# Kernel optimization log

Measured on AMD Instinct MI355X. Metric: run time of the kernel, lower is better.

Reference implementation:

```python
import jax, jax.numpy as jnp
import numpy as np

K = 2          # downsample rate
H = 8          # attention heads
D_LLM = 1024
DK = D_LLM // H
N_LAYER = 2
F_HID = D_LLM // 4  # 256, per PositionwiseFeedForward(llm_dim, llm_dim//4)
EPS = 1e-12


def _ln(x, g, b):
    m = jnp.mean(x, axis=-1, keepdims=True)
    v = jnp.mean((x - m) ** 2, axis=-1, keepdims=True)
    return (x - m) * jax.lax.rsqrt(v + EPS) * g + b


def setup_inputs() -> dict:
    key = jax.random.key(0)
    ks = jax.random.split(key, 16)
    s = 0.02
    d_in = 512 * K   # encoder_dim * k = 1024
    d_ff = 2048
    inp = {
        'x':  jax.random.normal(ks[0], (8, 2048, 512), dtype=jnp.float32),
        'W1': jax.random.normal(ks[1], (d_ff, d_in)) * s,
        'b1': jnp.zeros((d_ff,)),
        'W2': jax.random.normal(ks[2], (D_LLM, d_ff)) * s,
        'b2': jnp.zeros((D_LLM,)),
        'ln1_g': jnp.ones((N_LAYER, D_LLM)), 'ln1_b': jnp.zeros((N_LAYER, D_LLM)),
        'ln2_g': jnp.ones((N_LAYER, D_LLM)), 'ln2_b': jnp.zeros((N_LAYER, D_LLM)),
        'Wq': jax.random.normal(ks[3], (N_LAYER, D_LLM, D_LLM)) * s, 'bq': jnp.zeros((N_LAYER, D_LLM)),
        'Wk': jax.random.normal(ks[4], (N_LAYER, D_LLM, D_LLM)) * s, 'bk': jnp.zeros((N_LAYER, D_LLM)),
        'Wv': jax.random.normal(ks[5], (N_LAYER, D_LLM, D_LLM)) * s, 'bv': jnp.zeros((N_LAYER, D_LLM)),
        'Wo': jax.random.normal(ks[6], (N_LAYER, D_LLM, D_LLM)) * s, 'bo': jnp.zeros((N_LAYER, D_LLM)),
        'Fw1': jax.random.normal(ks[7], (N_LAYER, F_HID, D_LLM)) * s, 'Fb1': jnp.zeros((N_LAYER, F_HID)),
        'Fw2': jax.random.normal(ks[8], (N_LAYER, D_LLM, F_HID)) * s, 'Fb2': jnp.zeros((N_LAYER, D_LLM)),
    }
    return inp


def reference(x, W1, b1, W2, b2, ln1_g, ln1_b, ln2_g, ln2_b,
              Wq, bq, Wk, bk, Wv, bv, Wo, bo, Fw1, Fb1, Fw2, Fb2):
    B, S, D = x.shape
    chunk = (S - 1) // K + 1
    pad = chunk * K - S
    x = jnp.pad(x, ((0, 0), (0, pad), (0, 0)))
    x = x.reshape(B, chunk, K * D)                    # [B, T, k*D]
    # downsample projection: linear2(relu(linear1(x)))
    x = jax.nn.relu(x @ W1.T + b1) @ W2.T + b2        # [B, T, D_LLM]
    T = chunk
    for l in range(N_LAYER):
        # --- self-attention sublayer (pre-norm) ---
        resid = x
        h = _ln(x, ln1_g[l], ln1_b[l])
        q = (h @ Wq[l].T + bq[l]).reshape(B, T, H, DK).transpose(0, 2, 1, 3)
        k_ = (h @ Wk[l].T + bk[l]).reshape(B, T, H, DK).transpose(0, 2, 1, 3)
        v = (h @ Wv[l].T + bv[l]).reshape(B, T, H, DK).transpose(0, 2, 1, 3)
        scores = jnp.einsum('bhqd,bhkd->bhqk', q, k_) * (DK ** -0.5)
        attn = jax.nn.softmax(scores, axis=-1)        # mask is None
        o = jnp.einsum('bhqk,bhkd->bhqd', attn, v)
        o = o.transpose(0, 2, 1, 3).reshape(B, T, H * DK)
        x = resid + o @ Wo[l].T + bo[l]
        # --- FFN sublayer (pre-norm) ---
        resid = x
        h = _ln(x, ln2_g[l], ln2_b[l])
        x = resid + jax.nn.relu(h @ Fw1[l].T + Fb1[l]) @ Fw2[l].T + Fb2[l]
    return x
```

## Files before the change

### kernel.cpp

```cpp
#include <hip/hip_runtime.h>
#include <hip/hip_bf16.h>


#define DMODEL 1024
#define DFF 2048
#define FHID 256
#define NHEAD 8
#define DKH 128
#define TSEQ 1024

typedef __hip_bfloat16 bf16;
typedef __attribute__((ext_vector_type(8))) short bf16x8;
typedef __attribute__((ext_vector_type(4))) float f32x4;

#define MFMA16(a, b, c) __builtin_amdgcn_mfma_f32_16x16x32_bf16(a, b, c, 0, 0, 0)

__device__ int g_is_bf16;

__device__ __forceinline__ bool flagbf() {
    return __hip_atomic_load(&g_is_bf16, __ATOMIC_ACQUIRE,
                             __HIP_MEMORY_SCOPE_AGENT) != 0;
}
__device__ __forceinline__ bool flagbf_block() {
    __shared__ int fsh;
    if (threadIdx.x == 0)
        fsh = __hip_atomic_load(&g_is_bf16, __ATOMIC_ACQUIRE,
                                __HIP_MEMORY_SCOPE_AGENT);
    __syncthreads();
    return fsh != 0;
}
__device__ __forceinline__ float gload(const void* p, size_t i, bool bf) {
    return bf ? __bfloat162float(((const bf16*)p)[i]) : ((const float*)p)[i];
}
__device__ __forceinline__ void gstore(void* p, size_t i, bool bf, float v) {
    if (bf) ((bf16*)p)[i] = __float2bfloat16(v);
    else    ((float*)p)[i] = v;
}

__device__ __forceinline__ void async16(const bf16* g, const bf16* l) {
    __builtin_amdgcn_global_load_lds(
        (const __attribute__((address_space(1))) void*)g,
        (__attribute__((address_space(3))) void*)l, 16, 0, 0);
}

__global__ void detect_kernel(const void* __restrict__ probe) {
    const int lane = threadIdx.x & 63;
    const bf16* h = (const bf16*)probe;
    int ok = 1;
    #pragma unroll
    for (int j = 0; j < 4; ++j) {
        float v = __bfloat162float(h[lane * 4 + j]);
        if (!(fabsf(v) <= 1000.0f)) ok = 0;
    }
    unsigned long long m = __ballot(ok);
    if (lane == 0)
        __hip_atomic_store(&g_is_bf16, m == ~0ull ? 1 : 0, __ATOMIC_RELEASE,
                           __HIP_MEMORY_SCOPE_AGENT);
}

#define O_W1  0ull
#define O_W2  2097152ull
#define O_QK  4194304ull
#define O_WV  8388608ull
#define O_WO  10485760ull
#define O_F1  12582912ull
#define O_F2  13107200ull
#define ARENA_ELEMS 13631488ull

__global__ __launch_bounds__(256) void cvt_weights(
        const void* W1, const void* W2, const void* Wq, const void* Wk,
        const void* Wv, const void* Wo, const void* F1, const void* F2,
        bf16* __restrict__ arena) {
    if (flagbf_block()) return;
    int b = blockIdx.x;
    const float* src; bf16* dst;
    if      (b < 128)  {           src = (const float*)W1 + (size_t)b * 16384;
                         dst = arena + O_W1 + (size_t)b * 16384; }
    else if (b < 256)  { b -= 128; src = (const float*)W2 + (size_t)b * 16384;
                         dst = arena + O_W2 + (size_t)b * 16384; }
    else if (b < 384)  { b -= 256; src = (const float*)Wq + (size_t)b * 16384;
                         dst = arena + O_QK + (size_t)(b >> 6) * 2097152
                                            + (size_t)(b & 63) * 16384; }
    else if (b < 512)  { b -= 384; src = (const float*)Wk + (size_t)b * 16384;
                         dst = arena + O_QK + (size_t)(b >> 6) * 2097152
                                            + 1048576 + (size_t)(b & 63) * 16384; }
    else if (b < 640)  { b -= 512; src = (const float*)Wv + (size_t)b * 16384;
                         dst = arena + O_WV + (size_t)b * 16384; }
    else if (b < 768)  { b -= 640; src = (const float*)Wo + (size_t)b * 16384;
                         dst = arena + O_WO + (size_t)b * 16384; }
    else if (b < 800)  { b -= 768; src = (const float*)F1 + (size_t)b * 16384;
                         dst = arena + O_F1 + (size_t)b * 16384; }
    else               { b -= 800; src = (const float*)F2 + (size_t)b * 16384;
                         dst = arena + O_F2 + (size_t)b * 16384; }
    const int tid = threadIdx.x;
    #pragma unroll
    for (int it = 0; it < 16; ++it) {
        const int e = it * 1024 + tid * 4;
        float4 f = *(const float4*)(src + e);
        bf16 t[4] = {__float2bfloat16(f.x), __float2bfloat16(f.y),
                     __float2bfloat16(f.z), __float2bfloat16(f.w)};
        *(uint2*)(dst + e) = *(const uint2*)t;
    }
}

__global__ __launch_bounds__(256) void cvt_x(
        const void* __restrict__ X, size_t x_off, bf16* __restrict__ dst) {
    if (flagbf_block()) return;
    const float* src = (const float*)X + x_off + (size_t)blockIdx.x * 16384;
    bf16* d = dst + (size_t)blockIdx.x * 16384;
    const int tid = threadIdx.x;
    #pragma unroll
    for (int it = 0; it < 16; ++it) {
        const int e = it * 1024 + tid * 4;
        float4 f = *(const float4*)(src + e);
        bf16 t[4] = {__float2bfloat16(f.x), __float2bfloat16(f.y),
                     __float2bfloat16(f.z), __float2bfloat16(f.w)};
        *(uint2*)(d + e) = *(const uint2*)t;
    }
}

template <bool RELU, bool ADD, int CMODE, bool TRANSC, bool BIAS2>
__global__ __launch_bounds__(256) void gemm_bf16(
        const bf16* Abf, const bf16* Acv,
        const bf16* Wlo_bf, const bf16* Whi_bf,
        const bf16* Wlo_cv, const bf16* Whi_cv,
        const void* __restrict__ bias, const void* __restrict__ bias2,
        size_t b_off,
        void* __restrict__ C, size_t c_off,
        int M, int N, int K) {
    const bool fl = flagbf_block();
    const bf16* A   = fl ? Abf : Acv;
    const bf16* Wlo = fl ? Wlo_bf : Wlo_cv;
    const bf16* Whi = fl ? Whi_bf : Whi_cv;

    __shared__ __align__(16) bf16 As[128 * 64];
    __shared__ __align__(16) bf16 Bs[128 * 64];

    const int gx = gridDim.x;
    const int lin = blockIdx.x + gx * blockIdx.y;
    const int xcd = lin & 7, j = lin >> 3;
    const int rpx = gridDim.y >> 3;
    const int bm = (xcd * rpx + j / gx) * 128;
    const int bn = (j % gx) * 128;

    const int tid = threadIdx.x;
    const int wave = tid >> 6, lane = tid & 63;
    const int quad = lane >> 4, l15 = lane & 15;
    const int wr = wave >> 1, wc = wave & 1;
    const int l8 = lane >> 3, l7 = lane & 7;
    const int swz = l7 ^ l8;

    const bf16* Wp;
    int bnr;
    if (BIAS2 && bn >= 1024) { Wp = Whi; bnr = bn - 1024; }
    else                     { Wp = Wlo; bnr = bn; }

    f32x4 acc[4][4];
    #pragma unroll
    for (int i = 0; i < 4; ++i)
        #pragma unroll
        for (int j2 = 0; j2 < 4; ++j2) acc[i][j2] = (f32x4){0.f, 0.f, 0.f, 0.f};

    const bf16* ga0 = A  + (size_t)(bm  + wave * 32 + l8) * K + swz * 8;
    const bf16* gb0 = Wp + (size_t)(bnr + wave * 32 + l8) * K + swz * 8;
    bf16* la0 = &As[(wave * 32) * 64];
    bf16* lb0 = &Bs[(wave * 32) * 64];

    for (int k0 = 0; k0 < K; k0 += 64) {
        __syncthreads();
        #pragma unroll
        for (int i = 0; i < 4; ++i) {
            async16(ga0 + (size_t)(i * 8) * K + k0, la0 + i * 512);
            async16(gb0 + (size_t)(i * 8) * K + k0, lb0 + i * 512);
        }
        __syncthreads();

        #pragma unroll
        for (int ks = 0; ks < 2; ++ks) {
            bf16x8 af[4], bfr[4];
            #pragma unroll
            for (int mi = 0; mi < 4; ++mi) {
                const int row = wr * 64 + mi * 16 + l15;
                af[mi] = *(const bf16x8*)
                    &As[row * 64 + ((((ks << 2) | quad) ^ (row & 7)) << 3)];
            }
            #pragma unroll
            for (int ni = 0; ni < 4; ++ni) {
                const int row = wc * 64 + ni * 16 + l15;
                bfr[ni] = *(const bf16x8*)
                    &Bs[row * 64 + ((((ks << 2) | quad) ^ (row & 7)) << 3)];
            }
            #pragma unroll
            for (int mi = 0; mi < 4; ++mi)
                #pragma unroll
                for (int ni = 0; ni < 4; ++ni)
                    acc[mi][ni] = MFMA16(af[mi], bfr[ni], acc[mi][ni]);
        }
    }

    const bool cbf = CMODE ? fl : true;
    #pragma unroll
    for (int ni = 0; ni < 4; ++ni) {
        const int col = bn + wc * 64 + ni * 16 + l15;
        float bv;
        if (BIAS2) bv = col < 1024 ? gload(bias, b_off + col, fl)
                                   : gload(bias2, b_off + col - 1024, fl);
        else       bv = gload(bias, b_off + col, fl);
        #pragma unroll
        for (int mi = 0; mi < 4; ++mi) {
            const int row0 = bm + wr * 64 + mi * 16 + quad * 4;
            if (TRANSC) {
                bf16 pk[4];
                #pragma unroll
                for (int rr = 0; rr < 4; ++rr)
                    pk[rr] = __float2bfloat16(acc[mi][ni][rr] + bv);
                *(uint2*)((bf16*)C + c_off + (size_t)col * M + row0) =
                    *(const uint2*)pk;
            } else {
                #pragma unroll
                for (int rr = 0; rr < 4; ++rr) {
                    float v = acc[mi][ni][rr] + bv;
                    if (RELU) v = fmaxf(v, 0.f);
                    size_t idx = c_off + (size_t)(row0 + rr) * N + col;
                    if (ADD) v += gload(C, idx, cbf);
                    gstore(C, idx, cbf, v);
                }
            }
        }
    }
}

__global__ __launch_bounds__(256) void ln_wave(
        const void* __restrict__ X, size_t x_off,
        const void* __restrict__ g, const void* __restrict__ b, size_t gb_off,
        bf16* __restrict__ H) {
    const bool fl = flagbf_block();
    const int lane = threadIdx.x & 63;
    const int row = blockIdx.x * 4 + (threadIdx.x >> 6);
    const size_t xrow = x_off + (size_t)row * DMODEL;

    float v[16];
    if (fl) {
        const bf16* xp = (const bf16*)X + xrow;
        #pragma unroll
        for (int c = 0; c < 2; ++c) {
            uint4 raw = *(const uint4*)(xp + c * 512 + lane * 8);
            const bf16* rb = (const bf16*)&raw;
            #pragma unroll
            for (int j = 0; j < 8; ++j) v[c * 8 + j] = __bfloat162float(rb[j]);
        }
    } else {
        const float* xp = (const float*)X + xrow;
        #pragma unroll
        for (int c = 0; c < 4; ++c) {
            float4 f = *(const float4*)(xp + c * 256 + lane * 4);
            v[c * 4 + 0] = f.x; v[c * 4 + 1] = f.y;
            v[c * 4 + 2] = f.z; v[c * 4 + 3] = f.w;
        }
    }

    float s = 0.f;
    #pragma unroll
    for (int j = 0; j < 16; ++j) s += v[j];
    #pragma unroll
    for (int off = 32; off > 0; off >>= 1) s += __shfl_xor(s, off);
    const float mean = s * (1.f / DMODEL);

    float vs = 0.f;
    #pragma unroll
    for (int j = 0; j < 16; ++j) { float d = v[j] - mean; vs += d * d; }
    #pragma unroll
    for (int off = 32; off > 0; off >>= 1) vs += __shfl_xor(vs, off);
    const float rstd = rsqrtf(vs * (1.f / DMODEL) + 1e-12f);

    bf16* h = H + (size_t)row * DMODEL;
    if (fl) {
        const bf16* gp = (const bf16*)g + gb_off;
        const bf16* bp = (const bf16*)b + gb_off;
        #pragma unroll
        for (int c = 0; c < 2; ++c) {
            const int o = c * 512 + lane * 8;
            uint4 gr = *(const uint4*)(gp + o);
            uint4 br = *(const uint4*)(bp + o);
            const bf16* gg = (const bf16*)&gr;
            const bf16* bb = (const bf16*)&br;
            bf16 outv[8];
            #pragma unroll
            for (int j = 0; j < 8; ++j)
                outv[j] = __float2bfloat16((v[c * 8 + j] - mean) * rstd *
                          __bfloat162float(gg[j]) + __bfloat162float(bb[j]));
            *(uint4*)(h + o) = *(const uint4*)outv;
        }
    } else {
        const float* gp = (const float*)g + gb_off;
        const float* bp = (const float*)b + gb_off;
        #pragma unroll
        for (int c = 0; c < 4; ++c) {
            const int o = c * 256 + lane * 4;
            float4 gr = *(const float4*)(gp + o);
            float4 br = *(const float4*)(bp + o);
            const float gg[4] = {gr.x, gr.y, gr.z, gr.w};
            const float bb[4] = {br.x, br.y, br.z, br.w};
            bf16 outv[4];
            #pragma unroll
            for (int j = 0; j < 4; ++j)
                outv[j] = __float2bfloat16((v[c * 4 + j] - mean) * rstd * gg[j] + bb[j]);
            *(uint2*)(h + o) = *(const uint2*)outv;
        }
    }
}

__global__ __launch_bounds__(512) void attn_mfma(
        const bf16* __restrict__ QK, const bf16* __restrict__ Vg,
        bf16* __restrict__ Om) {
    const int cch = (int)gridDim.z;
    const int lin = blockIdx.x + (int)gridDim.x *
                    (blockIdx.y + (int)gridDim.y * blockIdx.z);
    const int xcd = lin & 7, j = lin >> 3;
    const int qt = j & 7, gl = j >> 3;
    const int g = xcd * cch + gl;
    const int h = g & 7, bb = g >> 3;

    const int Mc = cch * TSEQ;
    const int tid = threadIdx.x;
    const int wave = tid >> 6, lane = tid & 63;
    const int quad = lane >> 4, l15 = lane & 15;

    __shared__ __align__(16) bf16 Kt[64][128];
    __shared__ __align__(16) bf16 Vt[128][64];
    __shared__ __align__(16) bf16 Ps[8][16][72];

    const int qrow = qt * 128 + wave * 16 + l15;
    const float scale = 0.08838834764831845f;

    bf16x8 qf[4];
    #pragma unroll
    for (int kc = 0; kc < 4; ++kc) {
        uint4 raw = *(const uint4*)(QK + (size_t)(bb * TSEQ + qrow) * 2048 +
                                    h * DKH + kc * 32 + quad * 8);
        const bf16* rb = (const bf16*)&raw;
        bf16 tmp[8];
        #pragma unroll
        for (int j2 = 0; j2 < 8; ++j2)
            tmp[j2] = __float2bfloat16(__bfloat162float(rb[j2]) * scale);
        qf[kc] = *(const bf16x8*)tmp;
    }

    f32x4 o[8];
    #pragma unroll
    for (int i = 0; i < 8; ++i) o[i] = (f32x4){0.f, 0.f, 0.f, 0.f};
    float m_i[4] = {-1e30f, -1e30f, -1e30f, -1e30f};
    float l_i[4] = {0.f, 0.f, 0.f, 0.f};

    const int skey = tid >> 3;
    const int dseg = (tid & 7) * 16;
    const int sk7 = skey & 7;
    const int vd = tid >> 2;
    const int vseg = (tid & 3) * 16;

    for (int kt = 0; kt < TSEQ / 64; ++kt) {
        __syncthreads();
        {
            const bf16* kp = QK + (size_t)(bb * TSEQ + kt * 64 + skey) * 2048 +
                             1024 + h * DKH + dseg;
            const bf16* vp = Vg + (size_t)(h * DKH + vd) * Mc + bb * TSEQ +
                             kt * 64 + vseg;
            uint4 kv[2], vv[2];
            #pragma unroll
            for (int g2 = 0; g2 < 2; ++g2) { kv[g2] = ((const uint4*)kp)[g2]; vv[g2] = ((const uint4*)vp)[g2]; }
            #pragma unroll
            for (int g2 = 0; g2 < 2; ++g2) {
                int c = (dseg >> 3) + g2;
                *(uint4*)&Kt[skey][(c ^ sk7) << 3] = kv[g2];
            }
            #pragma unroll
            for (int g2 = 0; g2 < 2; ++g2) {
                int c = (vseg >> 3) + g2;
                *(uint4*)&Vt[vd][(c ^ (vd & 7)) << 3] = vv[g2];
            }
        }
        __syncthreads();

        f32x4 s[4];
        #pragma unroll
        for (int ni = 0; ni < 4; ++ni) s[ni] = (f32x4){0.f, 0.f, 0.f, 0.f};
        #pragma unroll
        for (int ni = 0; ni < 4; ++ni) {
            const int key = ni * 16 + l15;
            #pragma unroll
            for (int kc = 0; kc < 4; ++kc) {
                const int d3 = kc * 4 + quad;
                bf16x8 kb = *(const bf16x8*)&Kt[key][(d3 ^ (key & 7)) << 3];
                s[ni] = MFMA16(qf[kc], kb, s[ni]);
            }
        }

        float tm[4], ts[4];
        #pragma unroll
        for (int rr = 0; rr < 4; ++rr) {
            float v = fmaxf(fmaxf(s[0][rr], s[1][rr]), fmaxf(s[2][rr], s[3][rr]));
            v = fmaxf(v, __shfl_xor(v, 1));
            v = fmaxf(v, __shfl_xor(v, 2));
            v = fmaxf(v, __shfl_xor(v, 4));
            v = fmaxf(v, __shfl_xor(v, 8));
            tm[rr] = v;
        }
        int grow = 0;
        #pragma unroll
        for (int rr = 0; rr < 4; ++rr)
            grow |= (tm[rr] > m_i[rr] + 8.f) ? 1 : 0;
        if (__any(grow)) {
            float al[4];
            #pragma unroll
            for (int rr = 0; rr < 4; ++rr) {
                float mn = fmaxf(m_i[rr], tm[rr]);
                al[rr] = __expf(m_i[rr] - mn);
                m_i[rr] = mn;
                l_i[rr] *= al[rr];
            }
            #pragma unroll
            for (int i = 0; i < 8; ++i)
                #pragma unroll
                for (int rr = 0; rr < 4; ++rr) o[i][rr] *= al[rr];
        }
        #pragma unroll
        for (int rr = 0; rr < 4; ++rr) ts[rr] = 0.f;
        #pragma unroll
        for (int ni = 0; ni < 4; ++ni)
            #pragma unroll
            for (int rr = 0; rr < 4; ++rr) {
                float p = __expf(s[ni][rr] - m_i[rr]);
                s[ni][rr] = p;
                ts[rr] += p;
            }
        #pragma unroll
        for (int rr = 0; rr < 4; ++rr) {
            float v = ts[rr];
            v += __shfl_xor(v, 1);
            v += __shfl_xor(v, 2);
            v += __shfl_xor(v, 4);
            v += __shfl_xor(v, 8);
            l_i[rr] += v;
        }

        #pragma unroll
        for (int ni = 0; ni < 4; ++ni)
            #pragma unroll
            for (int rr = 0; rr < 4; ++rr)
                Ps[wave][quad * 4 + rr][ni * 16 + l15] = __float2bfloat16(s[ni][rr]);
        __asm__ __volatile__("s_waitcnt lgkmcnt(0)" ::: "memory");
        bf16x8 pa[2];
        #pragma unroll
        for (int kc2 = 0; kc2 < 2; ++kc2)
            pa[kc2] = *(const bf16x8*)&Ps[wave][l15][kc2 * 32 + quad * 8];

        #pragma unroll
        for (int ni2 = 0; ni2 < 8; ++ni2) {
            const int d = ni2 * 16 + l15;
            #pragma unroll
            for (int kc2 = 0; kc2 < 2; ++kc2) {
                const int key3 = kc2 * 4 + quad;
                bf16x8 vb = *(const bf16x8*)&Vt[d][(key3 ^ (d & 7)) << 3];
                o[ni2] = MFMA16(pa[kc2], vb, o[ni2]);
            }
        }
    }

    float rinv[4];
    #pragma unroll
    for (int rr = 0; rr < 4; ++rr) rinv[rr] = 1.0f / l_i[rr];
    const size_t obase = (size_t)bb * TSEQ * DMODEL + (size_t)h * DKH;
    #pragma unroll
    for (int ni2 = 0; ni2 < 8; ++ni2)
        #pragma unroll
        for (int rr = 0; rr < 4; ++rr) {
            int qr = qt * 128 + wave * 16 + quad * 4 + rr;
            Om[obase + (size_t)qr * DMODEL + ni2 * 16 + l15] =
                __float2bfloat16(o[ni2][rr] * rinv[rr]);
        }
}

extern "C" void kernel_launch(void* const* d_in, const int* in_sizes, int n_in,
                              void* d_out, int out_size, void* d_ws, size_t ws_size,
                              hipStream_t stream) {
    const void* x     = d_in[0];
    const void* W1    = d_in[1];
    const void* b1    = d_in[2];
    const void* W2    = d_in[3];
    const void* b2    = d_in[4];
    const void* ln1_g = d_in[5];
    const void* ln1_b = d_in[6];
    const void* ln2_g = d_in[7];
    const void* ln2_b = d_in[8];
    const void* Wq    = d_in[9];
    const void* bq    = d_in[10];
    const void* Wk    = d_in[11];
    const void* bk    = d_in[12];
    const void* Wv    = d_in[13];
    const void* bv    = d_in[14];
    const void* Wo    = d_in[15];
    const void* bo    = d_in[16];
    const void* Fw1   = d_in[17];
    const void* Fb1   = d_in[18];
    const void* Fw2   = d_in[19];
    const void* Fb2   = d_in[20];

    detect_kernel<<<1, 64, 0, stream>>>(W1);

    int c = 8;
    while (c > 1 &&
           (5ull * (size_t)c * (1ull << 20) + ARENA_ELEMS) * 2ull > ws_size)
        c >>= 1;
    const int nch = 8 / c;
    const int Mc = c * TSEQ;
    const size_t SL = (size_t)Mc * DMODEL;

    bf16* Hh  = (bf16*)d_ws;
    bf16* QKb = Hh + SL;
    bf16* Vtb = QKb + 2 * SL;
    bf16* Xc  = Vtb + SL;
    bf16* Wt  = Xc + SL;
    bf16* Hid = QKb;
    bf16* Ffh = QKb;
    bf16* Ob  = Hh;
    void* X = d_out;

    const bf16* xb  = (const bf16*)x;
    bf16* cW1  = Wt + O_W1;
    bf16* cW2  = Wt + O_W2;
    bf16* cWqk = Wt + O_QK;
    bf16* cWv  = Wt + O_WV;
    bf16* cWo  = Wt + O_WO;
    bf16* cF1  = Wt + O_F1;
    bf16* cF2  = Wt + O_F2;

    cvt_weights<<<832, 256, 0, stream>>>(W1, W2, Wq, Wk, Wv, Wo, Fw1, Fw2, Wt);

    for (int ci = 0; ci < nch; ++ci) {
        const size_t roff = (size_t)ci * Mc * DMODEL;

        cvt_x<<<(int)(SL / 16384), 256, 0, stream>>>(x, roff, Xc);

        gemm_bf16<true, false, 0, false, false><<<dim3(DFF / 128, Mc / 128), 256, 0, stream>>>(
            xb + roff, Xc, (const bf16*)W1, (const bf16*)W1, cW1, cW1,
            b1, nullptr, 0, Hid, 0, Mc, DFF, DMODEL);
        gemm_bf16<false, false, 1, false, false><<<dim3(DMODEL / 128, Mc / 128), 256, 0, stream>>>(
            Hid, Hid, (const bf16*)W2, (const bf16*)W2, cW2, cW2,
            b2, nullptr, 0, X, roff, Mc, DMODEL, DFF);

        for (int l = 0; l < 2; ++l) {
            const size_t wOff   = (size_t)l * DMODEL * DMODEL;
            const size_t fOff   = (size_t)l * FHID * DMODEL;
            const size_t vOff   = (size_t)l * DMODEL;
            const size_t f1bOff = (size_t)l * FHID;

            const bf16* wqL = (const bf16*)Wq + wOff;
            const bf16* wkL = (const bf16*)Wk + wOff;
            const bf16* wvL = (const bf16*)Wv + wOff;
            const bf16* woL = (const bf16*)Wo + wOff;
            const bf16* f1L = (const bf16*)Fw1 + fOff;
            const bf16* f2L = (const bf16*)Fw2 + fOff;
            const bf16* qkLo = cWqk + (size_t)l * 2097152;
            const bf16* qkHi = qkLo + 1048576;

            ln_wave<<<Mc / 4, 256, 0, stream>>>(X, roff, ln1_g, ln1_b, vOff, Hh);
            gemm_bf16<false, false, 0, false, true><<<dim3(2048 / 128, Mc / 128), 256, 0, stream>>>(
                Hh, Hh, wqL, wkL, qkLo, qkHi,
                bq, bk, vOff, QKb, 0, Mc, 2048, DMODEL);
            gemm_bf16<false, false, 0, true, false><<<dim3(DMODEL / 128, Mc / 128), 256, 0, stream>>>(
                Hh, Hh, wvL, wvL, cWv + wOff, cWv + wOff,
                bv, nullptr, vOff, Vtb, 0, Mc, DMODEL, DMODEL);

            attn_mfma<<<dim3(TSEQ / 128, NHEAD, c), 512, 0, stream>>>(QKb, Vtb, Ob);

            gemm_bf16<false, true, 1, false, false><<<dim3(DMODEL / 128, Mc / 128), 256, 0, stream>>>(
                Ob, Ob, woL, woL, cWo + wOff, cWo + wOff,
                bo, nullptr, vOff, X, roff, Mc, DMODEL, DMODEL);

            ln_wave<<<Mc / 4, 256, 0, stream>>>(X, roff, ln2_g, ln2_b, vOff, Hh);
            gemm_bf16<true, false, 0, false, false><<<dim3(FHID / 128, Mc / 128), 256, 0, stream>>>(
                Hh, Hh, f1L, f1L, cF1 + fOff, cF1 + fOff,
                Fb1, nullptr, f1bOff, Ffh, 0, Mc, FHID, DMODEL);
            gemm_bf16<false, true, 1, false, false><<<dim3(DMODEL / 128, Mc / 128), 256, 0, stream>>>(
                Ffh, Ffh, f2L, f2L, cF2 + fOff, cF2 + fOff,
                Fb2, nullptr, vOff, X, roff, Mc, DMODEL, FHID);
        }
    }
}
```

Before: 848.7 us.

## Add 256x128 double-buffered GEMM and register-prefetch K/V tiles in attention

Adds a new GEMM kernel with 256x128 block tiles, 512 threads, a K-step of 32 and double-buffered async LDS loads. It replaces the 128x128 GEMM for the downsample, QK, V and Wo projections. The attention kernel now prefetches the next K/V tile into registers while the current tile is computed, so global load latency overlaps with MFMA work. The cost is higher register pressure and a smaller grid, which means fewer blocks and possibly worse occupancy on some of the GEMMs.

```diff
diff --git a/kernel.cpp b/kernel.cpp
--- a/kernel.cpp
+++ b/kernel.cpp
@@ -17,10 +17,6 @@
 
 __device__ int g_is_bf16;
 
-__device__ __forceinline__ bool flagbf() {
-    return __hip_atomic_load(&g_is_bf16, __ATOMIC_ACQUIRE,
-                             __HIP_MEMORY_SCOPE_AGENT) != 0;
-}
 __device__ __forceinline__ bool flagbf_block() {
     __shared__ int fsh;
     if (threadIdx.x == 0)
@@ -120,6 +116,128 @@
 }
 
 template <bool RELU, bool ADD, int CMODE, bool TRANSC, bool BIAS2>
+__global__ __launch_bounds__(512, 4) void gemm256(
+        const bf16* Abf, const bf16* Acv,
+        const bf16* Wlo_bf, const bf16* Whi_bf,
+        const bf16* Wlo_cv, const bf16* Whi_cv,
+        const void* __restrict__ bias, const void* __restrict__ bias2,
+        size_t b_off,
+        void* __restrict__ C, size_t c_off,
+        int M, int N, int K) {
+    const bool fl = flagbf_block();
+    const bf16* A   = fl ? Abf : Acv;
+    const bf16* Wlo = fl ? Wlo_bf : Wlo_cv;
+    const bf16* Whi = fl ? Whi_bf : Whi_cv;
+
+    __shared__ __align__(16) bf16 As[2][256 * 32];
+    __shared__ __align__(16) bf16 Bs[2][128 * 32];
+
+    const int gx = gridDim.x;
+    const int lin = blockIdx.x + gx * blockIdx.y;
+    int bm, bn;
+    if ((gridDim.y & 7) == 0) {
+        const int xcd = lin & 7, j = lin >> 3;
+        const int rpx = gridDim.y >> 3;
+        bm = (xcd * rpx + (j / gx)) * 256;
+        bn = (j % gx) * 128;
+    } else {
+        bm = blockIdx.y * 256;
+        bn = blockIdx.x * 128;
+    }
+
+    const int tid = threadIdx.x;
+    const int wave = tid >> 6, lane = tid & 63;
+    const int quad = lane >> 4, l15 = lane & 15;
+    const int wm = wave >> 1, wn = wave & 1;
+
+    const bf16* Wp;
+    int bnr;
+    if (BIAS2 && bn >= 1024) { Wp = Whi; bnr = bn - 1024; }
+    else                     { Wp = Wlo; bnr = bn; }
+
+    const int srow = lane >> 2;
+    const int schunk = (lane & 3) ^ ((lane >> 3) & 3);
+    const bf16* gaBase = A  + (size_t)(bm  + wave * 32 + srow) * K + schunk * 8;
+    const bf16* gbBase = Wp + (size_t)(bnr + wave * 16 + srow) * K + schunk * 8;
+    const int laOff0 = (wave * 32) * 32;
+    const int laOff1 = (wave * 32 + 16) * 32;
+    const int lbOff  = (wave * 16) * 32;
+
+    f32x4 acc[4][4];
+    #pragma unroll
+    for (int i = 0; i < 4; ++i)
+        #pragma unroll
+        for (int j = 0; j < 4; ++j) acc[i][j] = (f32x4){0.f, 0.f, 0.f, 0.f};
+
+    const int nt = K >> 5;
+    int cur = 0;
+
+    async16(gaBase, &As[0][laOff0]);
+    async16(gaBase + (size_t)16 * K, &As[0][laOff1]);
+    async16(gbBase, &Bs[0][lbOff]);
+    __asm__ __volatile__("s_waitcnt vmcnt(0)" ::: "memory");
+    __syncthreads();
+
+    for (int t = 0; t < nt; ++t) {
+        if (t + 1 < nt) {
+            const int kn = (t + 1) << 5;
+            async16(gaBase + kn, &As[cur ^ 1][laOff0]);
+            async16(gaBase + (size_t)16 * K + kn, &As[cur ^ 1][laOff1]);
+            async16(gbBase + kn, &Bs[cur ^ 1][lbOff]);
+        }
+        bf16x8 bfr[4];
+        #pragma unroll
+        for (int ni = 0; ni < 4; ++ni) {
+            const int row = wn * 64 + ni * 16 + l15;
+            bfr[ni] = *(const bf16x8*)
+                &Bs[cur][row * 32 + ((quad ^ ((row >> 1) & 3)) << 3)];
+        }
+        #pragma unroll
+        for (int mi = 0; mi < 4; ++mi) {
+            const int row = wm * 64 + mi * 16 + l15;
+            bf16x8 af = *(const bf16x8*)
+                &As[cur][row * 32 + ((quad ^ ((row >> 1) & 3)) << 3)];
+            #pragma unroll
+            for (int ni = 0; ni < 4; ++ni)
+                acc[mi][ni] = MFMA16(af, bfr[ni], acc[mi][ni]);
+        }
+        __syncthreads();
+        cur ^= 1;
+    }
+
+    const bool cbf = CMODE ? fl : true;
+    #pragma unroll
+    for (int ni = 0; ni < 4; ++ni) {
+        const int col = bn + wn * 64 + ni * 16 + l15;
+        float bv;
+        if (BIAS2) bv = col < 1024 ? gload(bias, b_off + col, fl)
+                                   : gload(bias2, b_off + col - 1024, fl);
+        else       bv = gload(bias, b_off + col, fl);
+        #pragma unroll
+        for (int mi = 0; mi < 4; ++mi) {
+            const int row0 = bm + wm * 64 + mi * 16 + quad * 4;
+            if (TRANSC) {
+                bf16 pk[4];
+                #pragma unroll
+                for (int rr = 0; rr < 4; ++rr)
+                    pk[rr] = __float2bfloat16(acc[mi][ni][rr] + bv);
+                *(uint2*)((bf16*)C + c_off + (size_t)col * M + row0) =
+                    *(const uint2*)pk;
+            } else {
+                #pragma unroll
+                for (int rr = 0; rr < 4; ++rr) {
+                    float v = acc[mi][ni][rr] + bv;
+                    if (RELU) v = fmaxf(v, 0.f);
+                    size_t idx = c_off + (size_t)(row0 + rr) * N + col;
+                    if (ADD) v += gload(C, idx, cbf);
+                    gstore(C, idx, cbf, v);
+                }
+            }
+        }
+    }
+}
+
+template <bool RELU, bool ADD, int CMODE, bool TRANSC, bool BIAS2>
 __global__ __launch_bounds__(256) void gemm_bf16(
         const bf16* Abf, const bf16* Acv,
         const bf16* Wlo_bf, const bf16* Whi_bf,
@@ -138,10 +256,16 @@
 
     const int gx = gridDim.x;
     const int lin = blockIdx.x + gx * blockIdx.y;
-    const int xcd = lin & 7, j = lin >> 3;
-    const int rpx = gridDim.y >> 3;
-    const int bm = (xcd * rpx + j / gx) * 128;
-    const int bn = (j % gx) * 128;
+    int bm, bn;
+    if ((gridDim.y & 7) == 0) {
+        const int xcd = lin & 7, j = lin >> 3;
+        const int rpx = gridDim.y >> 3;
+        bm = (xcd * rpx + j / gx) * 128;
+        bn = (j % gx) * 128;
+    } else {
+        bm = blockIdx.y * 128;
+        bn = blockIdx.x * 128;
+    }
 
     const int tid = threadIdx.x;
     const int wave = tid >> 6, lane = tid & 63;
@@ -358,26 +482,27 @@
     const int vd = tid >> 2;
     const int vseg = (tid & 3) * 16;
 
-    for (int kt = 0; kt < TSEQ / 64; ++kt) {
+    const bf16* kRow = QK + (size_t)(bb * TSEQ + skey) * 2048 + 1024 +
+                       h * DKH + dseg;
+    const bf16* vRow = Vg + (size_t)(h * DKH + vd) * Mc + bb * TSEQ + vseg;
+
+    auto tile = [&](int kt, uint4& kI0, uint4& kI1, uint4& vI0, uint4& vI1,
+                    uint4& kO0, uint4& kO1, uint4& vO0, uint4& vO1, bool pf) {
         __syncthreads();
         {
-            const bf16* kp = QK + (size_t)(bb * TSEQ + kt * 64 + skey) * 2048 +
-                             1024 + h * DKH + dseg;
-            const bf16* vp = Vg + (size_t)(h * DKH + vd) * Mc + bb * TSEQ +
-                             kt * 64 + vseg;
-            uint4 kv[2], vv[2];
-            #pragma unroll
-            for (int g2 = 0; g2 < 2; ++g2) { kv[g2] = ((const uint4*)kp)[g2]; vv[g2] = ((const uint4*)vp)[g2]; }
-            #pragma unroll
-            for (int g2 = 0; g2 < 2; ++g2) {
-                int c = (dseg >> 3) + g2;
-                *(uint4*)&Kt[skey][(c ^ sk7) << 3] = kv[g2];
-            }
-            #pragma unroll
-            for (int g2 = 0; g2 < 2; ++g2) {
-                int c = (vseg >> 3) + g2;
-                *(uint4*)&Vt[vd][(c ^ (vd & 7)) << 3] = vv[g2];
-            }
+            const int c0 = dseg >> 3, d0 = vseg >> 3;
+            *(uint4*)&Kt[skey][((c0 + 0) ^ sk7) << 3] = kI0;
+            *(uint4*)&Kt[skey][((c0 + 1) ^ sk7) << 3] = kI1;
+            *(uint4*)&Vt[vd][((d0 + 0) ^ (vd & 7)) << 3] = vI0;
+            *(uint4*)&Vt[vd][((d0 + 1) ^ (vd & 7)) << 3] = vI1;
+        }
+        if (pf) {
+            const bf16* kp = kRow + (size_t)(kt + 1) * 64 * 2048;
+            const bf16* vp = vRow + (kt + 1) * 64;
+            kO0 = ((const uint4*)kp)[0];
+            kO1 = ((const uint4*)kp)[1];
+            vO0 = ((const uint4*)vp)[0];
+            vO1 = ((const uint4*)vp)[1];
         }
         __syncthreads();
 
@@ -464,6 +589,18 @@
                 o[ni2] = MFMA16(pa[kc2], vb, o[ni2]);
             }
         }
+    };
+
+    uint4 kA0, kA1, vA0, vA1, kB0, kB1, vB0, vB1;
+    kA0 = ((const uint4*)kRow)[0];
+    kA1 = ((const uint4*)kRow)[1];
+    vA0 = ((const uint4*)vRow)[0];
+    vA1 = ((const uint4*)vRow)[1];
+
+    #pragma unroll 1
+    for (int kt = 0; kt < TSEQ / 64; kt += 2) {
+        tile(kt,     kA0, kA1, vA0, vA1, kB0, kB1, vB0, vB1, true);
+        tile(kt + 1, kB0, kB1, vB0, vB1, kA0, kA1, vA0, vA1, kt + 2 < TSEQ / 64);
     }
 
     float rinv[4];
@@ -541,10 +678,10 @@
 
         cvt_x<<<(int)(SL / 16384), 256, 0, stream>>>(x, roff, Xc);
 
-        gemm_bf16<true, false, 0, false, false><<<dim3(DFF / 128, Mc / 128), 256, 0, stream>>>(
+        gemm256<true, false, 0, false, false><<<dim3(DFF / 128, Mc / 256), 512, 0, stream>>>(
             xb + roff, Xc, (const bf16*)W1, (const bf16*)W1, cW1, cW1,
             b1, nullptr, 0, Hid, 0, Mc, DFF, DMODEL);
-        gemm_bf16<false, false, 1, false, false><<<dim3(DMODEL / 128, Mc / 128), 256, 0, stream>>>(
+        gemm256<false, false, 1, false, false><<<dim3(DMODEL / 128, Mc / 256), 512, 0, stream>>>(
             Hid, Hid, (const bf16*)W2, (const bf16*)W2, cW2, cW2,
             b2, nullptr, 0, X, roff, Mc, DMODEL, DFF);
 
@@ -564,16 +701,16 @@
             const bf16* qkHi = qkLo + 1048576;
 
             ln_wave<<<Mc / 4, 256, 0, stream>>>(X, roff, ln1_g, ln1_b, vOff, Hh);
-            gemm_bf16<false, false, 0, false, true><<<dim3(2048 / 128, Mc / 128), 256, 0, stream>>>(
+            gemm256<false, false, 0, false, true><<<dim3(2048 / 128, Mc / 256), 512, 0, stream>>>(
                 Hh, Hh, wqL, wkL, qkLo, qkHi,
                 bq, bk, vOff, QKb, 0, Mc, 2048, DMODEL);
-            gemm_bf16<false, false, 0, true, false><<<dim3(DMODEL / 128, Mc / 128), 256, 0, stream>>>(
+            gemm256<false, false, 0, true, false><<<dim3(DMODEL / 128, Mc / 256), 512, 0, stream>>>(
                 Hh, Hh, wvL, wvL, cWv + wOff, cWv + wOff,
                 bv, nullptr, vOff, Vtb, 0, Mc, DMODEL, DMODEL);
 
             attn_mfma<<<dim3(TSEQ / 128, NHEAD, c), 512, 0, stream>>>(QKb, Vtb, Ob);
 
-            gemm_bf16<false, true, 1, false, false><<<dim3(DMODEL / 128, Mc / 128), 256, 0, stream>>>(
+            gemm256<false, true, 1, false, false><<<dim3(DMODEL / 128, Mc / 256), 512, 0, stream>>>(
                 Ob, Ob, woL, woL, cWo + wOff, cWo + wOff,
                 bo, nullptr, vOff, X, roff, Mc, DMODEL, DMODEL);
 
```

Result: slower. 867.0 us (+2.2%).
